# Optimization experiments

Measured on AMD Instinct MI355X. Metric: run time of the kernel, lower is better.

## Reference

```python
import jax, jax.numpy as jnp
import numpy as np

FEAT = 1024     # args.gl_text_dim
BERT_DIM = 768
EPS = 1e-12     # torch F.normalize eps


def _conv_branch(x, W, b):
    # x: (bs, L, 768); W: (FEAT, K, 768); b: (FEAT,)
    # Equivalent to Conv2d(1, FEAT, (K, 768)) then relu, already transposed to (bs, L-K+1, FEAT)
    K = W.shape[1]
    L = x.shape[1]
    out = sum(jnp.einsum('bld,fd->blf', x[:, k:L - K + 1 + k, :], W[:, k, :]) for k in range(K))
    return jax.nn.relu(out + b)


def _l2norm(x, axis):
    n = jnp.sqrt(jnp.sum(x * x, axis=axis, keepdims=True))
    return x / jnp.maximum(n, EPS)


def setup_inputs() -> dict:
    key = jax.random.key(0)
    ks = jax.random.split(key, 10)
    bs, L = 128, 128
    def w(k, shape, fan_in):
        bound = 1.0 / np.sqrt(fan_in)
        return jax.random.uniform(k, shape, jnp.float32, -bound, bound)
    return {
        'words_emb': jax.random.normal(ks[0], (bs, L, BERT_DIM), jnp.float32),
        'sent_emb': jax.random.normal(ks[1], (bs, BERT_DIM), jnp.float32),
        'W2': w(ks[2], (FEAT, 2, BERT_DIM), 2 * BERT_DIM), 'b2': w(ks[3], (FEAT,), 2 * BERT_DIM),
        'W3': w(ks[4], (FEAT, 3, BERT_DIM), 3 * BERT_DIM), 'b3': w(ks[5], (FEAT,), 3 * BERT_DIM),
        'W4': w(ks[6], (FEAT, 4, BERT_DIM), 4 * BERT_DIM), 'b4': w(ks[7], (FEAT,), 4 * BERT_DIM),
        'Wp': w(ks[8], (FEAT, BERT_DIM), BERT_DIM), 'bp': w(ks[9], (FEAT,), BERT_DIM),
    }


def reference(words_emb, sent_emb, W2, b2, W3, b3, W4, b4, Wp, bp):
    # sentence head: dropout(eval=identity) -> linear -> l2 normalize
    sent = _l2norm(sent_emb @ Wp.T + bp, axis=-1)  # (bs, FEAT)

    L = words_emb.shape[1]  # == bert_words_num
    a = _conv_branch(words_emb, W2, b2)  # (bs, L-1, FEAT)
    b_ = _conv_branch(words_emb, W3, b3)  # (bs, L-2, FEAT)
    c = _conv_branch(words_emb, W4, b4)  # (bs, L-3, FEAT)

    seq = L - 1 - 3  # args.bert_words_num - 1 - 3
    main = jnp.maximum(jnp.maximum(a[:, :seq], b_[:, :seq]), c[:, :seq])  # (bs, seq, FEAT)
    pen = jnp.maximum(a[:, seq], b_[:, seq])[:, None]                      # (bs, 1, FEAT)
    last = a[:, seq + 1][:, None]                                          # (bs, 1, FEAT)
    code = jnp.concatenate([main, pen, last], axis=1)                      # (bs, L-2, FEAT)
    code = _l2norm(code, axis=2)
    words_out = jnp.transpose(code, (0, 2, 1))                             # (bs, FEAT, L-2)
    return words_out, sent
```

## Files before the change

kernel.cpp:

```cpp
#include <hip/hip_runtime.h>
#include <math.h>

typedef unsigned short u16;

#define BSZ 128
#define SEQL 128
#define DIM 768
#define FEAT 1024
#define WORDS_OUT_ELEMS (BSZ * FEAT * 126)

typedef __attribute__((ext_vector_type(8))) __bf16 bf16x8;
typedef __attribute__((ext_vector_type(4))) float f32x4;

__device__ __forceinline__ u16 f2bf(float x) {
  unsigned u = __float_as_uint(x);
  u += 0x7FFFu + ((u >> 16) & 1u);
  return (u16)(u >> 16);
}

__device__ __forceinline__ void gld_lds16(const void* g, void* l) {
  __builtin_amdgcn_global_load_lds(
      (const __attribute__((address_space(1))) void*)g,
      (__attribute__((address_space(3))) void*)l, 16, 0, 0);
}

#define N4_WORDS 3145728
#define N4_W2 393216
#define N4_W3 589824
#define N4_W4 786432
#define N4_TOTAL (N4_WORDS + N4_W2 + N4_W3 + N4_W4)

__global__ __launch_bounds__(256) void cvt_all(const float* __restrict__ words,
                                               const float* __restrict__ W2,
                                               const float* __restrict__ W3,
                                               const float* __restrict__ W4,
                                               u16* __restrict__ dA, u16* __restrict__ d2,
                                               u16* __restrict__ d3, u16* __restrict__ d4) {
  int i = blockIdx.x * 256 + threadIdx.x;
  if (i >= N4_TOTAL) return;
  const float* src;
  u16* dst;
  int j = i;
  if (j < N4_WORDS) {
    src = words; dst = dA;
  } else if ((j -= N4_WORDS) < N4_W2) {
    src = W2; dst = d2;
  } else if ((j -= N4_W2) < N4_W3) {
    src = W3; dst = d3;
  } else {
    j -= N4_W3; src = W4; dst = d4;
  }
  float4 v = ((const float4*)src)[j];
  ushort4 o;
  o.x = f2bf(v.x); o.y = f2bf(v.y); o.z = f2bf(v.z); o.w = f2bf(v.w);
  ((ushort4*)dst)[j] = o;
}

__global__ __launch_bounds__(256) void gemm_fused(const u16* __restrict__ A,
                                                  const u16* __restrict__ W2,
                                                  const u16* __restrict__ W3,
                                                  const u16* __restrict__ W4,
                                                  const float* __restrict__ b2,
                                                  const float* __restrict__ b3,
                                                  const float* __restrict__ b4,
                                                  u16* __restrict__ Ca,
                                                  u16* __restrict__ Cb,
                                                  u16* __restrict__ Cc) {
  __shared__ u16 As[128 * 64];
  __shared__ u16 Bs[128 * 64];
  const int z = blockIdx.z;
  const int Lp = 127 - z;
  const int KD = 1536 + z * 768;
  const int tile_n = blockIdx.x;
  const int tile_m = blockIdx.y;
  if (tile_m >= Lp) return;

  const u16* W = (z == 0) ? W2 : (z == 1) ? W3 : W4;
  const float* bias = (z == 0) ? b2 : (z == 1) ? b3 : b4;
  u16* C = (z == 0) ? Ca : (z == 1) ? Cb : Cc;

  const int tid = threadIdx.x;
  const int wave = tid >> 6;
  const int lane = tid & 63;

  const int lr = lane >> 3;
  const int lc = lane & 7;
  const int lcol = (lc ^ (lr & 7)) * 8;
  const u16* ag[4];
  const u16* bg[4];
  unsigned lofs[4];
#pragma unroll
  for (int i = 0; i < 4; ++i) {
    int rl = wave * 32 + i * 8 + lr;
    int m = tile_m * 128 + rl;
    int bb = m / Lp;
    int ll = m - bb * Lp;
    ag[i] = A + (size_t)(bb * SEQL + ll) * DIM + lcol;
    int n = tile_n * 128 + rl;
    bg[i] = W + (size_t)n * KD + lcol;
    lofs[i] = __builtin_amdgcn_readfirstlane((unsigned)((wave * 32 + i * 8) * 64));
  }

  f32x4 acc[4][4];
#pragma unroll
  for (int mi = 0; mi < 4; ++mi)
#pragma unroll
    for (int ni = 0; ni < 4; ++ni) acc[mi][ni] = 0.0f;

  const int wm = (wave & 1) * 64;
  const int wn = (wave >> 1) * 64;
  const int frow = lane & 15;
  const int fq = lane >> 4;
  const int fsw = frow & 7;

  for (int k0 = 0; k0 < KD; k0 += 64) {
#pragma unroll
    for (int i = 0; i < 4; ++i) gld_lds16(ag[i] + k0, &As[lofs[i]]);
#pragma unroll
    for (int i = 0; i < 4; ++i) gld_lds16(bg[i] + k0, &Bs[lofs[i]]);
    __syncthreads();
#pragma unroll
    for (int kc = 0; kc < 2; ++kc) {
      const int csw = ((kc * 4 + fq) ^ fsw) * 8;
      bf16x8 af[4], bfr[4];
#pragma unroll
      for (int mi = 0; mi < 4; ++mi)
        af[mi] = *(const bf16x8*)&As[(wm + mi * 16 + frow) * 64 + csw];
#pragma unroll
      for (int ni = 0; ni < 4; ++ni)
        bfr[ni] = *(const bf16x8*)&Bs[(wn + ni * 16 + frow) * 64 + csw];
#pragma unroll
      for (int mi = 0; mi < 4; ++mi)
#pragma unroll
        for (int ni = 0; ni < 4; ++ni)
          acc[mi][ni] = __builtin_amdgcn_mfma_f32_16x16x32_bf16(af[mi], bfr[ni],
                                                                acc[mi][ni], 0, 0, 0);
    }
    __syncthreads();
  }

  float bv[4];
#pragma unroll
  for (int ni = 0; ni < 4; ++ni) bv[ni] = bias[tile_n * 128 + wn + ni * 16 + frow];
#pragma unroll
  for (int mi = 0; mi < 4; ++mi) {
#pragma unroll
    for (int r = 0; r < 4; ++r) {
      int mg = tile_m * 128 + wm + mi * 16 + fq * 4 + r;
      ushort4 hs;
      {
        float v0 = fmaxf(acc[mi][0][r] + bv[0], 0.0f);
        float v1 = fmaxf(acc[mi][1][r] + bv[1], 0.0f);
        float v2 = fmaxf(acc[mi][2][r] + bv[2], 0.0f);
        float v3 = fmaxf(acc[mi][3][r] + bv[3], 0.0f);
        hs.x = f2bf(v0); hs.y = f2bf(v1); hs.z = f2bf(v2); hs.w = f2bf(v3);
      }
      *(ushort4*)(C + (size_t)mg * FEAT + tile_n * 128 + wn + frow * 4) = hs;
    }
  }
}

__device__ __forceinline__ float4 load_bf4(const u16* p) {
  uint2 q = *(const uint2*)p;
  float4 r;
  r.x = __uint_as_float((q.x & 0xFFFFu) << 16);
  r.y = __uint_as_float(q.x & 0xFFFF0000u);
  r.z = __uint_as_float((q.y & 0xFFFFu) << 16);
  r.w = __uint_as_float(q.y & 0xFFFF0000u);
  return r;
}

__global__ __launch_bounds__(256) void combine_norm(const u16* __restrict__ a,
                                                    const u16* __restrict__ b,
                                                    const u16* __restrict__ c,
                                                    float* __restrict__ out) {
  __shared__ float comb[14 * 1024];
  __shared__ float red[14 * 4];
  __shared__ float inv[14];
  const int tid = threadIdx.x;
  const int wave = tid >> 6, lane = tid & 63;
  const int l0 = blockIdx.x * 14;
  const int bb = blockIdx.y;
  const int f0 = tid * 4;
  const int chunk = tid >> 4, frow = tid & 15;
  const int fbase = chunk * 64 + frow;

  float part[14];
#pragma unroll
  for (int l = 0; l < 14; ++l) {
    int lg = l0 + l;
    float4 v = load_bf4(a + (size_t)(bb * 127 + lg) * 1024 + f0);
    if (lg < 125) {
      float4 vb = load_bf4(b + (size_t)(bb * 126 + lg) * 1024 + f0);
      v.x = fmaxf(v.x, vb.x); v.y = fmaxf(v.y, vb.y);
      v.z = fmaxf(v.z, vb.z); v.w = fmaxf(v.w, vb.w);
    }
    if (lg < 124) {
      float4 vc = load_bf4(c + (size_t)(bb * 125 + lg) * 1024 + f0);
      v.x = fmaxf(v.x, vc.x); v.y = fmaxf(v.y, vc.y);
      v.z = fmaxf(v.z, vc.z); v.w = fmaxf(v.w, vc.w);
    }
    comb[l * 1024 + fbase + 0] = v.x;
    comb[l * 1024 + fbase + 16] = v.y;
    comb[l * 1024 + fbase + 32] = v.z;
    comb[l * 1024 + fbase + 48] = v.w;
    part[l] = v.x * v.x + v.y * v.y + v.z * v.z + v.w * v.w;
  }
#pragma unroll
  for (int l = 0; l < 14; ++l) {
    float v = part[l];
    for (int off = 32; off > 0; off >>= 1) v += __shfl_down(v, off);
    if (lane == 0) red[l * 4 + wave] = v;
  }
  __syncthreads();
  if (tid < 14) {
    float s = red[tid * 4] + red[tid * 4 + 1] + red[tid * 4 + 2] + red[tid * 4 + 3];
    inv[tid] = 1.0f / fmaxf(sqrtf(s), 1e-12f);
  }
  __syncthreads();

  const size_t ob = (size_t)bb * FEAT * 126;
#pragma unroll
  for (int it = 0; it < 4; ++it) {
    int f = tid + it * 256;
    float* po = out + ob + (size_t)f * 126 + l0;
#pragma unroll
    for (int j = 0; j < 7; ++j) {
      float2 w;
      w.x = comb[(2 * j) * 1024 + f] * inv[2 * j];
      w.y = comb[(2 * j + 1) * 1024 + f] * inv[2 * j + 1];
      *(float2*)(po + 2 * j) = w;
    }
  }
}

__global__ __launch_bounds__(256) void sent_head(const float* __restrict__ se,
                                                 const float* __restrict__ Wp,
                                                 const float* __restrict__ bp,
                                                 float* __restrict__ out) {
  __shared__ float srow[768];
  __shared__ float ov[1024];
  __shared__ float red[4];
  const int b = blockIdx.x, tid = threadIdx.x;
  for (int i = tid; i < 768; i += 256) srow[i] = se[b * 768 + i];
  __syncthreads();
  float ss = 0.f;
#pragma unroll
  for (int it = 0; it < 4; ++it) {
    int f = tid + it * 256;
    const float4* w = (const float4*)(Wp + (size_t)f * 768);
    float acc = 0.f;
    for (int j = 0; j < 192; ++j) {
      float4 wv = w[j];
      float4 sv = *(const float4*)&srow[j * 4];
      acc += wv.x * sv.x + wv.y * sv.y + wv.z * sv.z + wv.w * sv.w;
    }
    acc += bp[f];
    ov[f] = acc;
    ss += acc * acc;
  }
  const int lane = tid & 63, wave = tid >> 6;
  for (int off = 32; off > 0; off >>= 1) ss += __shfl_down(ss, off);
  if (lane == 0) red[wave] = ss;
  __syncthreads();
  float tot = red[0] + red[1] + red[2] + red[3];
  float inv = 1.0f / fmaxf(sqrtf(tot), 1e-12f);
  for (int it = 0; it < 4; ++it) {
    int f = tid + it * 256;
    out[WORDS_OUT_ELEMS + (size_t)b * 1024 + f] = ov[f] * inv;
  }
}

extern "C" void kernel_launch(void* const* d_in, const int* in_sizes, int n_in,
                              void* d_out, int out_size, void* d_ws, size_t ws_size,
                              hipStream_t stream) {
  const float* words = (const float*)d_in[0];
  const float* sent = (const float*)d_in[1];
  const float* W2 = (const float*)d_in[2];
  const float* b2 = (const float*)d_in[3];
  const float* W3 = (const float*)d_in[4];
  const float* b3 = (const float*)d_in[5];
  const float* W4 = (const float*)d_in[6];
  const float* b4 = (const float*)d_in[7];
  const float* Wp = (const float*)d_in[8];
  const float* bp = (const float*)d_in[9];
  float* out = (float*)d_out;

  char* ws = (char*)d_ws;
  u16* A_bf = (u16*)(ws + 0);
  u16* W2_bf = (u16*)(ws + 25165824);
  u16* W3_bf = (u16*)(ws + 28311552);
  u16* W4_bf = (u16*)(ws + 33030144);
  u16* a_out = (u16*)(ws + 39321600);
  u16* b_out = (u16*)(ws + 72613888);
  u16* c_out = (u16*)(ws + 105644032);

  cvt_all<<<(N4_TOTAL + 255) / 256, 256, 0, stream>>>(words, W2, W3, W4,
                                                      A_bf, W2_bf, W3_bf, W4_bf);

  gemm_fused<<<dim3(8, 127, 3), 256, 0, stream>>>(A_bf, W2_bf, W3_bf, W4_bf,
                                                  b2, b3, b4, a_out, b_out, c_out);

  combine_norm<<<dim3(9, BSZ), 256, 0, stream>>>(a_out, b_out, c_out, out);
  sent_head<<<BSZ, 256, 0, stream>>>(sent, Wp, bp, out);
}
```

Baseline: 584.9 us.

## Restructure conv GEMM per batch to reuse input tile across kernel taps

Each block of the conv GEMM now handles one batch sample and one N-tile for one branch. It stages a 128x64 slice of that sample's word embeddings in LDS once and reuses it for every conv tap by shifting the row index, instead of gathering im2col rows of length K*768 from global memory. The weight slices for successive taps are double-buffered so the next tap's load overlaps the current tap's MFMAs. The cost is a larger LDS footprint (48KB), which may lower occupancy, and a sync after every tap. Fragment rows past the staged tile read into the weight buffer, but they only feed output rows that are masked off.

```diff
diff --git a/kernel.cpp b/kernel.cpp
--- a/kernel.cpp
+++ b/kernel.cpp
@@ -56,6 +56,100 @@
   ((ushort4*)dst)[j] = o;
 }
 
+
+__device__ __forceinline__ void stage_tile(const u16* __restrict__ gbase, int stride,
+                                           u16* __restrict__ ldsbase, int wave, int lane) {
+#pragma unroll
+  for (int i = 0; i < 4; ++i) {
+    int slot = i * 256 + wave * 64 + lane;
+    int r = slot >> 3, c = slot & 7;
+    const u16* src = gbase + (size_t)r * stride + ((c ^ (r & 7)) * 8);
+    unsigned uofs = __builtin_amdgcn_readfirstlane((unsigned)((i * 256 + wave * 64) * 8));
+    gld_lds16(src, ldsbase + uofs);
+  }
+}
+
+template <int K>
+__device__ __forceinline__ void run_branch(const u16* __restrict__ A,
+                                           const u16* __restrict__ W,
+                                           const float* __restrict__ bias,
+                                           u16* __restrict__ C,
+                                           int b, int tile_n, u16* lds) {
+  const int KD = K * 768;
+  const int Lp = 129 - K;
+  const int tid = threadIdx.x;
+  const int wave = tid >> 6, lane = tid & 63;
+  u16* Xs = lds;
+  u16* Wb0 = lds + 8192;
+  u16* Wb1 = lds + 16384;
+
+  const int wm = (wave & 1) * 64;
+  const int wn = (wave >> 1) * 64;
+  const int frow = lane & 15;
+  const int fq = lane >> 4;
+
+  const u16* xg = A + (size_t)b * 128 * 768;
+  const u16* wg = W + (size_t)tile_n * 128 * KD;
+
+  f32x4 acc[4][4];
+#pragma unroll
+  for (int mi = 0; mi < 4; ++mi)
+#pragma unroll
+    for (int ni = 0; ni < 4; ++ni) acc[mi][ni] = 0.0f;
+
+  for (int d0 = 0; d0 < 768; d0 += 64) {
+    stage_tile(xg + d0, 768, Xs, wave, lane);
+    stage_tile(wg + d0, KD, Wb0, wave, lane);
+    __syncthreads();
+#pragma unroll
+    for (int k = 0; k < K; ++k) {
+      if (k + 1 < K)
+        stage_tile(wg + (k + 1) * 768 + d0, KD, ((k + 1) & 1) ? Wb1 : Wb0, wave, lane);
+      const u16* wbuf = (k & 1) ? Wb1 : Wb0;
+#pragma unroll
+      for (int kc = 0; kc < 2; ++kc) {
+        bf16x8 af[4], wf[4];
+#pragma unroll
+        for (int mi = 0; mi < 4; ++mi) {
+          int row = wm + mi * 16 + frow + k;
+          af[mi] = *(const bf16x8*)&Xs[(row * 8 + ((kc * 4 + fq) ^ (row & 7))) * 8];
+        }
+#pragma unroll
+        for (int ni = 0; ni < 4; ++ni) {
+          int row = wn + ni * 16 + frow;
+          wf[ni] = *(const bf16x8*)&wbuf[(row * 8 + ((kc * 4 + fq) ^ (row & 7))) * 8];
+        }
+#pragma unroll
+        for (int mi = 0; mi < 4; ++mi)
+#pragma unroll
+          for (int ni = 0; ni < 4; ++ni)
+            acc[mi][ni] = __builtin_amdgcn_mfma_f32_16x16x32_bf16(af[mi], wf[ni],
+                                                                  acc[mi][ni], 0, 0, 0);
+      }
+      __syncthreads();
+    }
+  }
+
+  float bv[4];
+#pragma unroll
+  for (int ni = 0; ni < 4; ++ni) bv[ni] = bias[tile_n * 128 + wn + ni * 16 + frow];
+#pragma unroll
+  for (int mi = 0; mi < 4; ++mi) {
+#pragma unroll
+    for (int r = 0; r < 4; ++r) {
+      int mg = wm + mi * 16 + fq * 4 + r;
+      if (mg < Lp) {
+        ushort4 hs;
+        hs.x = f2bf(fmaxf(acc[mi][0][r] + bv[0], 0.0f));
+        hs.y = f2bf(fmaxf(acc[mi][1][r] + bv[1], 0.0f));
+        hs.z = f2bf(fmaxf(acc[mi][2][r] + bv[2], 0.0f));
+        hs.w = f2bf(fmaxf(acc[mi][3][r] + bv[3], 0.0f));
+        *(ushort4*)(C + (size_t)(b * Lp + mg) * FEAT + tile_n * 128 + wn + frow * 4) = hs;
+      }
+    }
+  }
+}
+
 __global__ __launch_bounds__(256) void gemm_fused(const u16* __restrict__ A,
                                                   const u16* __restrict__ W2,
                                                   const u16* __restrict__ W3,
@@ -66,98 +160,16 @@
                                                   u16* __restrict__ Ca,
                                                   u16* __restrict__ Cb,
                                                   u16* __restrict__ Cc) {
-  __shared__ u16 As[128 * 64];
-  __shared__ u16 Bs[128 * 64];
-  const int z = blockIdx.z;
-  const int Lp = 127 - z;
-  const int KD = 1536 + z * 768;
+  __shared__ u16 lds[24576];
   const int tile_n = blockIdx.x;
-  const int tile_m = blockIdx.y;
-  if (tile_m >= Lp) return;
-
-  const u16* W = (z == 0) ? W2 : (z == 1) ? W3 : W4;
-  const float* bias = (z == 0) ? b2 : (z == 1) ? b3 : b4;
-  u16* C = (z == 0) ? Ca : (z == 1) ? Cb : Cc;
-
-  const int tid = threadIdx.x;
-  const int wave = tid >> 6;
-  const int lane = tid & 63;
-
-  const int lr = lane >> 3;
-  const int lc = lane & 7;
-  const int lcol = (lc ^ (lr & 7)) * 8;
-  const u16* ag[4];
-  const u16* bg[4];
-  unsigned lofs[4];
-#pragma unroll
-  for (int i = 0; i < 4; ++i) {
-    int rl = wave * 32 + i * 8 + lr;
-    int m = tile_m * 128 + rl;
-    int bb = m / Lp;
-    int ll = m - bb * Lp;
-    ag[i] = A + (size_t)(bb * SEQL + ll) * DIM + lcol;
-    int n = tile_n * 128 + rl;
-    bg[i] = W + (size_t)n * KD + lcol;
-    lofs[i] = __builtin_amdgcn_readfirstlane((unsigned)((wave * 32 + i * 8) * 64));
-  }
-
-  f32x4 acc[4][4];
-#pragma unroll
-  for (int mi = 0; mi < 4; ++mi)
-#pragma unroll
-    for (int ni = 0; ni < 4; ++ni) acc[mi][ni] = 0.0f;
-
-  const int wm = (wave & 1) * 64;
-  const int wn = (wave >> 1) * 64;
-  const int frow = lane & 15;
-  const int fq = lane >> 4;
-  const int fsw = frow & 7;
-
-  for (int k0 = 0; k0 < KD; k0 += 64) {
-#pragma unroll
-    for (int i = 0; i < 4; ++i) gld_lds16(ag[i] + k0, &As[lofs[i]]);
-#pragma unroll
-    for (int i = 0; i < 4; ++i) gld_lds16(bg[i] + k0, &Bs[lofs[i]]);
-    __syncthreads();
-#pragma unroll
-    for (int kc = 0; kc < 2; ++kc) {
-      const int csw = ((kc * 4 + fq) ^ fsw) * 8;
-      bf16x8 af[4], bfr[4];
-#pragma unroll
-      for (int mi = 0; mi < 4; ++mi)
-        af[mi] = *(const bf16x8*)&As[(wm + mi * 16 + frow) * 64 + csw];
-#pragma unroll
-      for (int ni = 0; ni < 4; ++ni)
-        bfr[ni] = *(const bf16x8*)&Bs[(wn + ni * 16 + frow) * 64 + csw];
-#pragma unroll
-      for (int mi = 0; mi < 4; ++mi)
-#pragma unroll
-        for (int ni = 0; ni < 4; ++ni)
-          acc[mi][ni] = __builtin_amdgcn_mfma_f32_16x16x32_bf16(af[mi], bfr[ni],
-                                                                acc[mi][ni], 0, 0, 0);
-    }
-    __syncthreads();
-  }
-
-  float bv[4];
-#pragma unroll
-  for (int ni = 0; ni < 4; ++ni) bv[ni] = bias[tile_n * 128 + wn + ni * 16 + frow];
-#pragma unroll
-  for (int mi = 0; mi < 4; ++mi) {
-#pragma unroll
-    for (int r = 0; r < 4; ++r) {
-      int mg = tile_m * 128 + wm + mi * 16 + fq * 4 + r;
-      ushort4 hs;
-      {
-        float v0 = fmaxf(acc[mi][0][r] + bv[0], 0.0f);
-        float v1 = fmaxf(acc[mi][1][r] + bv[1], 0.0f);
-        float v2 = fmaxf(acc[mi][2][r] + bv[2], 0.0f);
-        float v3 = fmaxf(acc[mi][3][r] + bv[3], 0.0f);
-        hs.x = f2bf(v0); hs.y = f2bf(v1); hs.z = f2bf(v2); hs.w = f2bf(v3);
-      }
-      *(ushort4*)(C + (size_t)mg * FEAT + tile_n * 128 + wn + frow * 4) = hs;
-    }
-  }
+  const int z = blockIdx.y;
+  const int b = blockIdx.z;
+  if (z == 0)
+    run_branch<2>(A, W2, b2, Ca, b, tile_n, lds);
+  else if (z == 1)
+    run_branch<3>(A, W3, b3, Cb, b, tile_n, lds);
+  else
+    run_branch<4>(A, W4, b4, Cc, b, tile_n, lds);
 }
 
 __device__ __forceinline__ float4 load_bf4(const u16* p) {
@@ -298,7 +310,7 @@
   cvt_all<<<(N4_TOTAL + 255) / 256, 256, 0, stream>>>(words, W2, W3, W4,
                                                       A_bf, W2_bf, W3_bf, W4_bf);
 
-  gemm_fused<<<dim3(8, 127, 3), 256, 0, stream>>>(A_bf, W2_bf, W3_bf, W4_bf,
+  gemm_fused<<<dim3(8, 3, BSZ), 256, 0, stream>>>(A_bf, W2_bf, W3_bf, W4_bf,
                                                   b2, b3, b4, a_out, b_out, c_out);
 
   combine_norm<<<dim3(9, BSZ), 256, 0, stream>>>(a_out, b_out, c_out, out);
```

Result: faster. 521.9 us (-10.8%).
